# Kernel tuning notes

Measured on AMD Instinct MI355X. Metric: run time of the kernel, lower is better.

## Reference

```python
import jax, jax.numpy as jnp
import numpy as np

N = 100000        # nodes
E = 1600000       # directed edges (avg degree 16)
F_IN, F_HID, F_OUT = 512, 32, 16


def setup_inputs() -> dict:
    key = jax.random.key(0)
    k0, k1, k2, k3 = jax.random.split(key, 4)
    x = jax.random.normal(k0, (N, F_IN), dtype=jnp.float32)
    edge_index = jax.random.randint(k1, (2, E), 0, N, dtype=jnp.int32)
    # Glorot-ish init for the two GCNConv linear weights
    W1 = jax.random.normal(k2, (F_IN, F_HID), dtype=jnp.float32) / np.float32(np.sqrt(F_IN))
    W2 = jax.random.normal(k3, (F_HID, F_OUT), dtype=jnp.float32) / np.float32(np.sqrt(F_HID))
    b1 = jnp.zeros((F_HID,), jnp.float32)
    b2 = jnp.zeros((F_OUT,), jnp.float32)
    return {"x": x, "W1": W1, "b1": b1, "W2": W2, "b2": b2, "edge_index": edge_index}


def gcn_conv(x, W, b, src, dst):
    """PyG GCNConv: h = x W; symmetric-normalized aggregation with self-loops; + bias."""
    h = x @ W                                   # [N, F_out] project first (PyG order)
    # degree including the implicit self-loop (start from ones)
    deg = jnp.ones((N,), h.dtype).at[dst].add(1.0)
    dinv = jax.lax.rsqrt(deg)                   # deg^{-1/2}
    coef = (dinv[src] * dinv[dst])[:, None]     # [E, 1] edge norm
    msg = h[src] * coef                         # gather + scale
    agg = jax.ops.segment_sum(msg, dst, num_segments=N)  # scatter-add to dst
    agg = agg + h * (dinv * dinv)[:, None]      # self-loop contribution
    return agg + b


def reference(x, W1, b1, W2, b2, edge_index):
    src, dst = edge_index[0], edge_index[1]
    h = jax.nn.relu(gcn_conv(x, W1, b1, src, dst))
    # F.dropout(training=self.training) is identity in eval mode
    h = gcn_conv(h, W2, b2, src, dst)
    return jax.nn.log_softmax(h, axis=1)
```

## Files before the change

kernel.cpp:

```cpp
#include <hip/hip_runtime.h>
#include <hip/hip_bf16.h>
#include <cstdint>

#define NN   100000
#define NE   1600000
#define FIN  512
#define FHID 32
#define FOUT 16

#define BSHIFT 8
#define BSIZE  256
#define NBUCK  391
#define EPB    2048
#define NCHUNK ((NE + EPB - 1) / EPB)
#define GROWS  64
#define GB     ((NN + GROWS - 1) / GROWS)

typedef float f32x4 __attribute__((ext_vector_type(4)));
typedef short s16x8 __attribute__((ext_vector_type(8)));
typedef short s16x4 __attribute__((ext_vector_type(4)));
typedef int   i32x4 __attribute__((ext_vector_type(4)));
typedef unsigned int u32;
typedef unsigned short u16;

__device__ __forceinline__ short f2bf(float f) {
  union { float f; uint32_t u; } v; v.f = f;
  uint32_t r = v.u + 0x7fffu + ((v.u >> 16) & 1u);
  return (short)(r >> 16);
}
__device__ __forceinline__ float bf2f(u16 u) {
  union { uint32_t u; float f; } v; v.u = (uint32_t)u << 16; return v.f;
}

__global__ __launch_bounds__(256) void k_hist(const int* __restrict__ dst,
                                              u32* __restrict__ bcount) {
  __shared__ u32 h[NBUCK];
  int tid = threadIdx.x;
  for (int i = tid; i < NBUCK; i += 256) h[i] = 0;
  __syncthreads();
  int base = blockIdx.x * EPB;
  #pragma unroll
  for (int i = 0; i < 2; ++i) {
    int e0 = base + (i * 256 + tid) * 4;
    if (e0 + 3 < NE) {
      i32x4 d4 = *(const i32x4*)(dst + e0);
      atomicAdd(&h[d4[0] >> BSHIFT], 1u);
      atomicAdd(&h[d4[1] >> BSHIFT], 1u);
      atomicAdd(&h[d4[2] >> BSHIFT], 1u);
      atomicAdd(&h[d4[3] >> BSHIFT], 1u);
    } else {
      for (int k = 0; k < 4; ++k)
        if (e0 + k < NE) atomicAdd(&h[dst[e0 + k] >> BSHIFT], 1u);
    }
  }
  __syncthreads();
  for (int i = tid; i < NBUCK; i += 256)
    if (h[i]) atomicAdd(&bcount[i], h[i]);
}

__global__ __launch_bounds__(512) void k_bscan(const u32* __restrict__ bc,
                                               u32* __restrict__ bstart,
                                               u32* __restrict__ bcur,
                                               const float* __restrict__ W1,
                                               u16* __restrict__ wfrag) {
  __shared__ u32 tmp[512];
  int tid = threadIdx.x;
  u32 v = (tid < NBUCK) ? bc[tid] : 0;
  tmp[tid] = v;
  __syncthreads();
  #pragma unroll
  for (int off = 1; off < 512; off <<= 1) {
    u32 t = (tid >= off) ? tmp[tid - off] : 0;
    __syncthreads();
    tmp[tid] += t;
    __syncthreads();
  }
  if (tid < NBUCK) { u32 e = tmp[tid] - v; bstart[tid] = e; bcur[tid] = e; }
  if (tid == 511) bstart[NBUCK] = tmp[511];

  for (int it = 0; it < 32; ++it) {
    int flat = it * 512 + tid;
    int i  = flat & 7;
    int l  = (flat >> 3) & 63;
    int nt = (flat >> 9) & 1;
    int kt = flat >> 10;
    int k  = kt * 32 + ((l >> 4) << 3) + i;
    int n  = nt * 16 + (l & 15);
    wfrag[flat] = (u16)f2bf(W1[k * 32 + n]);
  }
}

__global__ __launch_bounds__(512) void k_bin(const int* __restrict__ src,
                                             const int* __restrict__ dst,
                                             u32* __restrict__ bcur,
                                             u32* __restrict__ binned) {
  __shared__ u32 cnt[NBUCK];
  __shared__ u32 lofs[NBUCK];
  __shared__ u32 gbase[NBUCK];
  __shared__ u32 tmp[512];
  __shared__ u32 stage[EPB];
  __shared__ u16 sb[EPB];
  int tid = threadIdx.x;
  for (int i = tid; i < NBUCK; i += 512) cnt[i] = 0;
  __syncthreads();

  int base = blockIdx.x * EPB;
  int e0 = base + tid * 4;
  u32 vals[4]; u32 ofs[4]; int bks[4];
  if (e0 + 3 < NE) {
    i32x4 s4 = *(const i32x4*)(src + e0);
    i32x4 d4 = *(const i32x4*)(dst + e0);
    #pragma unroll
    for (int k = 0; k < 4; ++k) {
      int b = d4[k] >> BSHIFT;
      bks[k] = b;
      vals[k] = (u32)s4[k] | ((u32)(d4[k] & (BSIZE - 1)) << 17);
      ofs[k] = atomicAdd(&cnt[b], 1u);
    }
  } else {
    #pragma unroll
    for (int k = 0; k < 4; ++k) {
      int e = e0 + k;
      bool ok = e < NE;
      int s = 0, d = 0;
      if (ok) { s = src[e]; d = dst[e]; }
      int b = ok ? (d >> BSHIFT) : -1;
      bks[k] = b;
      vals[k] = (u32)s | ((u32)(d & (BSIZE - 1)) << 17);
      ofs[k] = ok ? atomicAdd(&cnt[b], 1u) : 0;
    }
  }
  __syncthreads();

  u32 cv = (tid < NBUCK) ? cnt[tid] : 0;
  tmp[tid] = cv;
  __syncthreads();
  #pragma unroll
  for (int off = 1; off < 512; off <<= 1) {
    u32 t = (tid >= off) ? tmp[tid - off] : 0;
    __syncthreads();
    tmp[tid] += t;
    __syncthreads();
  }
  if (tid < NBUCK) {
    lofs[tid] = tmp[tid] - cv;
    gbase[tid] = cv ? atomicAdd(&bcur[tid], cv) : 0;
  }
  __syncthreads();
  u32 total = tmp[511];
  __syncthreads();

  #pragma unroll
  for (int k = 0; k < 4; ++k) {
    if (bks[k] >= 0) {
      u32 sl = lofs[bks[k]] + ofs[k];
      stage[sl] = vals[k];
      sb[sl] = (u16)bks[k];
    }
  }
  __syncthreads();

  for (u32 s2 = tid; s2 < total; s2 += 512) {
    int b = sb[s2];
    binned[gbase[b] + (s2 - lofs[b])] = stage[s2];
  }
}

__global__ __launch_bounds__(256) void k_fin(const u32* __restrict__ binned,
                                             const u32* __restrict__ bstart,
                                             int* __restrict__ deg,
                                             int* __restrict__ rs,
                                             float* __restrict__ dinv,
                                             int* __restrict__ csr) {
  __shared__ u32 degl[BSIZE];
  __shared__ u32 rsl[BSIZE];
  int tid = threadIdx.x;
  int b = blockIdx.x;
  u32 start = bstart[b];
  u32 n = bstart[b + 1] - start;

  degl[tid] = 0;
  __syncthreads();
  for (u32 k = tid; k < n; k += 256)
    atomicAdd(&degl[binned[start + k] >> 17], 1u);
  __syncthreads();

  u32 v = degl[tid];
  rsl[tid] = v;
  __syncthreads();
  #pragma unroll
  for (int off = 1; off < 256; off <<= 1) {
    u32 t = (tid >= off) ? rsl[tid - off] : 0;
    __syncthreads();
    rsl[tid] += t;
    __syncthreads();
  }
  u32 e = rsl[tid] - v;
  __syncthreads();
  rsl[tid] = e;

  int g = b * BSIZE + tid;
  if (g < NN) {
    deg[g] = (int)v;
    rs[g] = (int)(start + e);
    dinv[g] = rsqrtf(1.0f + (float)v);
  }
  __syncthreads();

  for (u32 k = tid; k < n; k += 256) {
    u32 vv = binned[start + k];
    u32 pos = atomicAdd(&rsl[vv >> 17], 1u);
    csr[start + pos] = (int)(vv & 0x1FFFFu);
  }
}

__global__ __launch_bounds__(256) void k_gemm1(const float* __restrict__ x,
                                               const u16* __restrict__ wfrag,
                                               const float* __restrict__ dinv,
                                               u16* __restrict__ Hs1) {
  __shared__ u16 Xs[4][16][512];
  const int tid  = threadIdx.x;
  const int lane = tid & 63;
  const int wv   = tid >> 6;
  const int r0   = blockIdx.x * GROWS + wv * 16;
  char* xw = (char*)&Xs[wv][0][0];

  #pragma unroll
  for (int bat = 0; bat < 2; ++bat) {
    f32x4 va[8], vb[8];
    #pragma unroll
    for (int r = 0; r < 8; ++r) {
      int row = r0 + bat * 8 + r;
      if (row >= NN) row = NN - 1;
      const float* rp = x + (size_t)row * FIN;
      va[r] = *(const f32x4*)(rp + lane * 4);
      vb[r] = *(const f32x4*)(rp + 256 + lane * 4);
    }
    #pragma unroll
    for (int r = 0; r < 8; ++r) {
      int rr = bat * 8 + r;
      u32 sw = (u32)((rr & 7) << 4);
      s16x4 w0, w1;
      #pragma unroll
      for (int q = 0; q < 4; ++q) { w0[q] = f2bf(va[r][q]); w1[q] = f2bf(vb[r][q]); }
      *(s16x4*)(xw + (((u32)(rr * 1024 + lane * 8)) ^ sw))       = w0;
      *(s16x4*)(xw + (((u32)(rr * 1024 + 512 + lane * 8)) ^ sw)) = w1;
    }
  }

  const int h = lane >> 4;
  const int m = lane & 15;
  const u32 msw = (u32)((m & 7) << 4);
  const s16x8* wf = (const s16x8*)wfrag;
  f32x4 acc0 = {}, acc1 = {};
  #pragma unroll
  for (int kt = 0; kt < 16; ++kt) {
    s16x8 af = *(const s16x8*)(xw + (((u32)(m * 1024 + kt * 64 + h * 16)) ^ msw));
    s16x8 b0 = wf[(kt * 2 + 0) * 64 + lane];
    s16x8 b1 = wf[(kt * 2 + 1) * 64 + lane];
    acc0 = __builtin_amdgcn_mfma_f32_16x16x32_bf16(af, b0, acc0, 0, 0, 0);
    acc1 = __builtin_amdgcn_mfma_f32_16x16x32_bf16(af, b1, acc1, 0, 0, 0);
  }
  #pragma unroll
  for (int r = 0; r < 4; ++r) {
    int row = r0 + h * 4 + r;
    if (row < NN) {
      float di = dinv[row];
      u16* o = Hs1 + (size_t)row * FHID + m;
      o[0]  = (u16)f2bf(acc0[r] * di);
      o[16] = (u16)f2bf(acc1[r] * di);
    }
  }
}

__global__ __launch_bounds__(256) void k_gat1(const int* __restrict__ csr,
                                              const int* __restrict__ rs,
                                              const int* __restrict__ deg,
                                              const float* __restrict__ dinv,
                                              const float* __restrict__ b1,
                                              const float* __restrict__ W2,
                                              const u16* __restrict__ Hs1,
                                              u16* __restrict__ Hs2) {
  __shared__ float w[FHID * FOUT];
  for (int i = threadIdx.x; i < FHID * FOUT; i += 256) w[i] = W2[i];
  __syncthreads();

  int t = blockIdx.x * 256 + threadIdx.x;
  int d = t >> 2;
  if (d >= NN) return;
  int p = t & 3;
  int start = rs[d], n = deg[d];

  float a0[8], a1[8], a2[8], a3[8];
  {
    s16x8 v = *(const s16x8*)(Hs1 + (size_t)d * FHID + p * 8);
    #pragma unroll
    for (int k = 0; k < 8; ++k) {
      a0[k] = bf2f((u16)v[k]); a1[k] = 0.f; a2[k] = 0.f; a3[k] = 0.f;
    }
  }
  int j = 0;
  for (; j + 8 <= n; j += 8) {
    int s0=csr[start+j],   s1=csr[start+j+1], s2=csr[start+j+2], s3=csr[start+j+3];
    int s4=csr[start+j+4], s5=csr[start+j+5], s6=csr[start+j+6], s7=csr[start+j+7];
    s16x8 v0 = *(const s16x8*)(Hs1 + (size_t)s0 * FHID + p * 8);
    s16x8 v1 = *(const s16x8*)(Hs1 + (size_t)s1 * FHID + p * 8);
    s16x8 v2 = *(const s16x8*)(Hs1 + (size_t)s2 * FHID + p * 8);
    s16x8 v3 = *(const s16x8*)(Hs1 + (size_t)s3 * FHID + p * 8);
    s16x8 v4 = *(const s16x8*)(Hs1 + (size_t)s4 * FHID + p * 8);
    s16x8 v5 = *(const s16x8*)(Hs1 + (size_t)s5 * FHID + p * 8);
    s16x8 v6 = *(const s16x8*)(Hs1 + (size_t)s6 * FHID + p * 8);
    s16x8 v7 = *(const s16x8*)(Hs1 + (size_t)s7 * FHID + p * 8);
    #pragma unroll
    for (int k = 0; k < 8; ++k) {
      a0[k] += bf2f((u16)v0[k]);
      a1[k] += bf2f((u16)v1[k]);
      a2[k] += bf2f((u16)v2[k]);
      a3[k] += bf2f((u16)v3[k]);
      a0[k] += bf2f((u16)v4[k]);
      a1[k] += bf2f((u16)v5[k]);
      a2[k] += bf2f((u16)v6[k]);
      a3[k] += bf2f((u16)v7[k]);
    }
  }
  for (; j + 4 <= n; j += 4) {
    int s0=csr[start+j], s1=csr[start+j+1], s2=csr[start+j+2], s3=csr[start+j+3];
    s16x8 v0 = *(const s16x8*)(Hs1 + (size_t)s0 * FHID + p * 8);
    s16x8 v1 = *(const s16x8*)(Hs1 + (size_t)s1 * FHID + p * 8);
    s16x8 v2 = *(const s16x8*)(Hs1 + (size_t)s2 * FHID + p * 8);
    s16x8 v3 = *(const s16x8*)(Hs1 + (size_t)s3 * FHID + p * 8);
    #pragma unroll
    for (int k = 0; k < 8; ++k) {
      a0[k] += bf2f((u16)v0[k]);
      a1[k] += bf2f((u16)v1[k]);
      a2[k] += bf2f((u16)v2[k]);
      a3[k] += bf2f((u16)v3[k]);
    }
  }
  for (; j < n; ++j) {
    int s0 = csr[start + j];
    s16x8 v0 = *(const s16x8*)(Hs1 + (size_t)s0 * FHID + p * 8);
    #pragma unroll
    for (int k = 0; k < 8; ++k) a0[k] += bf2f((u16)v0[k]);
  }

  float dd = dinv[d];
  float h[8];
  #pragma unroll
  for (int k = 0; k < 8; ++k)
    h[k] = fmaxf(((a0[k] + a1[k]) + (a2[k] + a3[k])) * dd + b1[p * 8 + k], 0.0f);

  float pj[FOUT];
  #pragma unroll
  for (int jj = 0; jj < FOUT; ++jj) pj[jj] = 0.f;
  #pragma unroll
  for (int k = 0; k < 8; ++k)
    #pragma unroll
    for (int jj = 0; jj < FOUT; ++jj)
      pj[jj] = fmaf(h[k], w[(p * 8 + k) * FOUT + jj], pj[jj]);
  #pragma unroll
  for (int jj = 0; jj < FOUT; ++jj) {
    pj[jj] += __shfl_xor(pj[jj], 1);
    pj[jj] += __shfl_xor(pj[jj], 2);
  }
  s16x4 o;
  #pragma unroll
  for (int q = 0; q < 4; ++q) o[q] = f2bf(pj[p * 4 + q] * dd);
  *(s16x4*)(Hs2 + (size_t)d * FOUT + p * 4) = o;
}

__global__ __launch_bounds__(256) void k_gat2(const int* __restrict__ csr,
                                              const int* __restrict__ rs,
                                              const int* __restrict__ deg,
                                              const float* __restrict__ dinv,
                                              const float* __restrict__ b2,
                                              const u16* __restrict__ Hs2,
                                              float* __restrict__ out) {
  int t = blockIdx.x * 256 + threadIdx.x;
  int d = t >> 2;
  if (d >= NN) return;
  int p = t & 3;
  int start = rs[d], n = deg[d];

  float a0[4], a1[4], a2[4], a3[4];
  {
    s16x4 v = *(const s16x4*)(Hs2 + (size_t)d * FOUT + p * 4);
    #pragma unroll
    for (int k = 0; k < 4; ++k) { a0[k] = bf2f((u16)v[k]); a1[k]=0.f; a2[k]=0.f; a3[k]=0.f; }
  }
  int j = 0;
  for (; j + 8 <= n; j += 8) {
    int s0=csr[start+j],   s1=csr[start+j+1], s2=csr[start+j+2], s3=csr[start+j+3];
    int s4=csr[start+j+4], s5=csr[start+j+5], s6=csr[start+j+6], s7=csr[start+j+7];
    s16x4 v0 = *(const s16x4*)(Hs2 + (size_t)s0 * FOUT + p * 4);
    s16x4 v1 = *(const s16x4*)(Hs2 + (size_t)s1 * FOUT + p * 4);
    s16x4 v2 = *(const s16x4*)(Hs2 + (size_t)s2 * FOUT + p * 4);
    s16x4 v3 = *(const s16x4*)(Hs2 + (size_t)s3 * FOUT + p * 4);
    s16x4 v4 = *(const s16x4*)(Hs2 + (size_t)s4 * FOUT + p * 4);
    s16x4 v5 = *(const s16x4*)(Hs2 + (size_t)s5 * FOUT + p * 4);
    s16x4 v6 = *(const s16x4*)(Hs2 + (size_t)s6 * FOUT + p * 4);
    s16x4 v7 = *(const s16x4*)(Hs2 + (size_t)s7 * FOUT + p * 4);
    #pragma unroll
    for (int k = 0; k < 4; ++k) {
      a0[k] += bf2f((u16)v0[k]); a1[k] += bf2f((u16)v1[k]);
      a2[k] += bf2f((u16)v2[k]); a3[k] += bf2f((u16)v3[k]);
      a0[k] += bf2f((u16)v4[k]); a1[k] += bf2f((u16)v5[k]);
      a2[k] += bf2f((u16)v6[k]); a3[k] += bf2f((u16)v7[k]);
    }
  }
  for (; j + 4 <= n; j += 4) {
    int s0=csr[start+j], s1=csr[start+j+1], s2=csr[start+j+2], s3=csr[start+j+3];
    s16x4 v0 = *(const s16x4*)(Hs2 + (size_t)s0 * FOUT + p * 4);
    s16x4 v1 = *(const s16x4*)(Hs2 + (size_t)s1 * FOUT + p * 4);
    s16x4 v2 = *(const s16x4*)(Hs2 + (size_t)s2 * FOUT + p * 4);
    s16x4 v3 = *(const s16x4*)(Hs2 + (size_t)s3 * FOUT + p * 4);
    #pragma unroll
    for (int k = 0; k < 4; ++k) {
      a0[k] += bf2f((u16)v0[k]); a1[k] += bf2f((u16)v1[k]);
      a2[k] += bf2f((u16)v2[k]); a3[k] += bf2f((u16)v3[k]);
    }
  }
  for (; j < n; ++j) {
    int s0 = csr[start + j];
    s16x4 v0 = *(const s16x4*)(Hs2 + (size_t)s0 * FOUT + p * 4);
    #pragma unroll
    for (int k = 0; k < 4; ++k) a0[k] += bf2f((u16)v0[k]);
  }

  float dd = dinv[d];
  float z[4];
  #pragma unroll
  for (int k = 0; k < 4; ++k)
    z[k] = ((a0[k]+a1[k]) + (a2[k]+a3[k])) * dd + b2[p * 4 + k];

  float m = fmaxf(fmaxf(z[0], z[1]), fmaxf(z[2], z[3]));
  m = fmaxf(m, __shfl_xor(m, 1));
  m = fmaxf(m, __shfl_xor(m, 2));
  float s = expf(z[0]-m) + expf(z[1]-m) + expf(z[2]-m) + expf(z[3]-m);
  s += __shfl_xor(s, 1);
  s += __shfl_xor(s, 2);
  float lse = m + logf(s);

  f32x4 o = { z[0]-lse, z[1]-lse, z[2]-lse, z[3]-lse };
  *(f32x4*)(out + (size_t)d * FOUT + p * 4) = o;
}

extern "C" void kernel_launch(void* const* d_in, const int* in_sizes, int n_in,
                              void* d_out, int out_size, void* d_ws, size_t ws_size,
                              hipStream_t stream) {
  const float* x  = (const float*)d_in[0];
  const float* W1 = (const float*)d_in[1];
  const float* b1 = (const float*)d_in[2];
  const float* W2 = (const float*)d_in[3];
  const float* b2 = (const float*)d_in[4];
  const int*   ei = (const int*)d_in[5];
  const int* srcv = ei;
  const int* dstv = ei + NE;

  char* ws = (char*)d_ws;
  const size_t KB = 1024, MB = 1048576;
  u32*   bcount = (u32*)(ws + 0);
  u32*   bstart = (u32*)(ws + 8 * KB);
  u32*   bcur   = (u32*)(ws + 16 * KB);
  u16*   wfrag  = (u16*)(ws + 64 * KB);
  int*   deg    = (int*)(ws + 512 * KB);
  int*   rs     = (int*)(ws + 1024 * KB);
  float* dinv   = (float*)(ws + 1536 * KB);
  u32*   binned = (u32*)(ws + 2 * MB);
  int*   csr    = (int*)(ws + 9 * MB);
  u16*   Hs1    = (u16*)(ws + 16 * MB);
  u16*   Hs2    = (u16*)(ws + 23 * MB);
  float* out    = (float*)d_out;

  hipMemsetAsync(bcount, 0, NBUCK * sizeof(u32), stream);

  k_hist <<<NCHUNK, 256, 0, stream>>>(dstv, bcount);
  k_bscan<<<1,      512, 0, stream>>>(bcount, bstart, bcur, W1, wfrag);
  k_bin  <<<NCHUNK, 512, 0, stream>>>(srcv, dstv, bcur, binned);
  k_fin  <<<NBUCK,  256, 0, stream>>>(binned, bstart, deg, rs, dinv, csr);
  k_gemm1<<<GB, 256, 0, stream>>>(x, wfrag, dinv, Hs1);
  k_gat1 <<<(NN * 4 + 255) / 256, 256, 0, stream>>>(csr, rs, deg, dinv, b1, W2, Hs1, Hs2);
  k_gat2 <<<(NN * 4 + 255) / 256, 256, 0, stream>>>(csr, rs, deg, dinv, b2, Hs2, out);
}
```

Measured before the change: 155.2 us.

## Pipeline GEMM1 tiles per wave and enlarge histogram/binning work per block

The feature GEMM now has each wave process two 16-row tiles: it issues the global loads for the second tile before running MFMA on the first, so memory latency overlaps compute, and the grid halves to 782 blocks. The histogram becomes a grid-stride loop over 128 blocks, cutting the number of global atomic merges. Binning handles 4096 edges per block with 8 edges per thread, giving fewer blocks and fewer global bucket-cursor atomics. The costs are higher register pressure in GEMM (16+16 f32x4 held live), more shared memory in binning, and less parallelism in the histogram. The histogram loop also drops the tail path, which is only safe because NE is a multiple of 4.

Measured after the change: 139.2 us. 10.3% less time.

```diff
diff --git a/kernel.cpp b/kernel.cpp
--- a/kernel.cpp
+++ b/kernel.cpp
@@ -11,10 +11,10 @@
 #define BSHIFT 8
 #define BSIZE  256
 #define NBUCK  391
-#define EPB    2048
-#define NCHUNK ((NE + EPB - 1) / EPB)
-#define GROWS  64
-#define GB     ((NN + GROWS - 1) / GROWS)
+#define HB     128
+#define BEPB   4096
+#define NBB    ((NE + BEPB - 1) / BEPB)
+#define GB     782
 
 typedef float f32x4 __attribute__((ext_vector_type(4)));
 typedef short s16x8 __attribute__((ext_vector_type(8)));
@@ -38,20 +38,13 @@
   int tid = threadIdx.x;
   for (int i = tid; i < NBUCK; i += 256) h[i] = 0;
   __syncthreads();
-  int base = blockIdx.x * EPB;
-  #pragma unroll
-  for (int i = 0; i < 2; ++i) {
-    int e0 = base + (i * 256 + tid) * 4;
-    if (e0 + 3 < NE) {
-      i32x4 d4 = *(const i32x4*)(dst + e0);
-      atomicAdd(&h[d4[0] >> BSHIFT], 1u);
-      atomicAdd(&h[d4[1] >> BSHIFT], 1u);
-      atomicAdd(&h[d4[2] >> BSHIFT], 1u);
-      atomicAdd(&h[d4[3] >> BSHIFT], 1u);
-    } else {
-      for (int k = 0; k < 4; ++k)
-        if (e0 + k < NE) atomicAdd(&h[dst[e0 + k] >> BSHIFT], 1u);
-    }
+  const int stride = HB * 256 * 4;
+  for (int e0 = (blockIdx.x * 256 + tid) * 4; e0 + 3 < NE; e0 += stride) {
+    i32x4 d4 = *(const i32x4*)(dst + e0);
+    atomicAdd(&h[d4[0] >> BSHIFT], 1u);
+    atomicAdd(&h[d4[1] >> BSHIFT], 1u);
+    atomicAdd(&h[d4[2] >> BSHIFT], 1u);
+    atomicAdd(&h[d4[3] >> BSHIFT], 1u);
   }
   __syncthreads();
   for (int i = tid; i < NBUCK; i += 256)
@@ -98,36 +91,39 @@
   __shared__ u32 lofs[NBUCK];
   __shared__ u32 gbase[NBUCK];
   __shared__ u32 tmp[512];
-  __shared__ u32 stage[EPB];
-  __shared__ u16 sb[EPB];
+  __shared__ u32 stage[BEPB];
+  __shared__ u16 sb[BEPB];
   int tid = threadIdx.x;
   for (int i = tid; i < NBUCK; i += 512) cnt[i] = 0;
   __syncthreads();
 
-  int base = blockIdx.x * EPB;
-  int e0 = base + tid * 4;
-  u32 vals[4]; u32 ofs[4]; int bks[4];
-  if (e0 + 3 < NE) {
-    i32x4 s4 = *(const i32x4*)(src + e0);
-    i32x4 d4 = *(const i32x4*)(dst + e0);
-    #pragma unroll
-    for (int k = 0; k < 4; ++k) {
-      int b = d4[k] >> BSHIFT;
-      bks[k] = b;
-      vals[k] = (u32)s4[k] | ((u32)(d4[k] & (BSIZE - 1)) << 17);
-      ofs[k] = atomicAdd(&cnt[b], 1u);
-    }
-  } else {
-    #pragma unroll
-    for (int k = 0; k < 4; ++k) {
-      int e = e0 + k;
-      bool ok = e < NE;
-      int s = 0, d = 0;
-      if (ok) { s = src[e]; d = dst[e]; }
-      int b = ok ? (d >> BSHIFT) : -1;
-      bks[k] = b;
-      vals[k] = (u32)s | ((u32)(d & (BSIZE - 1)) << 17);
-      ofs[k] = ok ? atomicAdd(&cnt[b], 1u) : 0;
+  int base = blockIdx.x * BEPB;
+  u32 vals[8]; u32 ofs[8]; int bks[8];
+  #pragma unroll
+  for (int half = 0; half < 2; ++half) {
+    int e0 = base + tid * 8 + half * 4;
+    if (e0 + 3 < NE) {
+      i32x4 s4 = *(const i32x4*)(src + e0);
+      i32x4 d4 = *(const i32x4*)(dst + e0);
+      #pragma unroll
+      for (int k = 0; k < 4; ++k) {
+        int b = d4[k] >> BSHIFT;
+        bks[half * 4 + k] = b;
+        vals[half * 4 + k] = (u32)s4[k] | ((u32)(d4[k] & (BSIZE - 1)) << 17);
+        ofs[half * 4 + k] = atomicAdd(&cnt[b], 1u);
+      }
+    } else {
+      #pragma unroll
+      for (int k = 0; k < 4; ++k) {
+        int e = e0 + k;
+        bool ok = e < NE;
+        int s = 0, d = 0;
+        if (ok) { s = src[e]; d = dst[e]; }
+        int b = ok ? (d >> BSHIFT) : -1;
+        bks[half * 4 + k] = b;
+        vals[half * 4 + k] = (u32)s | ((u32)(d & (BSIZE - 1)) << 17);
+        ofs[half * 4 + k] = ok ? atomicAdd(&cnt[b], 1u) : 0;
+      }
     }
   }
   __syncthreads();
@@ -151,7 +147,7 @@
   __syncthreads();
 
   #pragma unroll
-  for (int k = 0; k < 4; ++k) {
+  for (int k = 0; k < 8; ++k) {
     if (bks[k] >= 0) {
       u32 sl = lofs[bks[k]] + ofs[k];
       stage[sl] = vals[k];
@@ -214,6 +210,60 @@
   }
 }
 
+#define G1_ISSUE(TILE)                                                        \
+  do {                                                                        \
+    int r0_ = (TILE) * 16;                                                    \
+    _Pragma("unroll")                                                         \
+    for (int r_ = 0; r_ < 16; ++r_) {                                         \
+      int row_ = r0_ + r_;                                                    \
+      if (row_ >= NN) row_ = NN - 1;                                          \
+      const float* rp_ = x + (size_t)row_ * FIN + lane * 4;                   \
+      va[r_] = *(const f32x4*)rp_;                                            \
+      vb[r_] = *(const f32x4*)(rp_ + 256);                                    \
+    }                                                                         \
+  } while (0)
+
+#define G1_CVTWRITE()                                                         \
+  do {                                                                        \
+    _Pragma("unroll")                                                         \
+    for (int r_ = 0; r_ < 16; ++r_) {                                         \
+      u32 sw_ = (u32)((r_ & 7) << 4);                                         \
+      s16x4 w0_, w1_;                                                         \
+      _Pragma("unroll")                                                       \
+      for (int q_ = 0; q_ < 4; ++q_) {                                        \
+        w0_[q_] = f2bf(va[r_][q_]);                                           \
+        w1_[q_] = f2bf(vb[r_][q_]);                                           \
+      }                                                                       \
+      *(s16x4*)(xw + (((u32)(r_ * 1024 + lane * 8)) ^ sw_)) = w0_;            \
+      *(s16x4*)(xw + (((u32)(r_ * 1024 + 512 + lane * 8)) ^ sw_)) = w1_;      \
+    }                                                                         \
+  } while (0)
+
+#define G1_MFMA_STORE(TILE)                                                   \
+  do {                                                                        \
+    f32x4 acc0_ = {}, acc1_ = {};                                             \
+    _Pragma("unroll")                                                         \
+    for (int kt_ = 0; kt_ < 16; ++kt_) {                                      \
+      s16x8 af_ = *(const s16x8*)(xw +                                        \
+          (((u32)(m * 1024 + kt_ * 64 + h * 16)) ^ msw));                     \
+      s16x8 b0_ = wf[(kt_ * 2 + 0) * 64 + lane];                              \
+      s16x8 b1_ = wf[(kt_ * 2 + 1) * 64 + lane];                              \
+      acc0_ = __builtin_amdgcn_mfma_f32_16x16x32_bf16(af_, b0_, acc0_, 0,0,0);\
+      acc1_ = __builtin_amdgcn_mfma_f32_16x16x32_bf16(af_, b1_, acc1_, 0,0,0);\
+    }                                                                         \
+    int r0_ = (TILE) * 16;                                                    \
+    _Pragma("unroll")                                                         \
+    for (int r_ = 0; r_ < 4; ++r_) {                                          \
+      int row_ = r0_ + h * 4 + r_;                                            \
+      if (row_ < NN) {                                                        \
+        float di_ = dinv[row_];                                               \
+        u16* o_ = Hs1 + (size_t)row_ * FHID + m;                              \
+        o_[0]  = (u16)f2bf(acc0_[r_] * di_);                                  \
+        o_[16] = (u16)f2bf(acc1_[r_] * di_);                                  \
+      }                                                                       \
+    }                                                                         \
+  } while (0)
+
 __global__ __launch_bounds__(256) void k_gemm1(const float* __restrict__ x,
                                                const u16* __restrict__ wfrag,
                                                const float* __restrict__ dinv,
@@ -222,55 +272,21 @@
   const int tid  = threadIdx.x;
   const int lane = tid & 63;
   const int wv   = tid >> 6;
-  const int r0   = blockIdx.x * GROWS + wv * 16;
   char* xw = (char*)&Xs[wv][0][0];
-
-  #pragma unroll
-  for (int bat = 0; bat < 2; ++bat) {
-    f32x4 va[8], vb[8];
-    #pragma unroll
-    for (int r = 0; r < 8; ++r) {
-      int row = r0 + bat * 8 + r;
-      if (row >= NN) row = NN - 1;
-      const float* rp = x + (size_t)row * FIN;
-      va[r] = *(const f32x4*)(rp + lane * 4);
-      vb[r] = *(const f32x4*)(rp + 256 + lane * 4);
-    }
-    #pragma unroll
-    for (int r = 0; r < 8; ++r) {
-      int rr = bat * 8 + r;
-      u32 sw = (u32)((rr & 7) << 4);
-      s16x4 w0, w1;
-      #pragma unroll
-      for (int q = 0; q < 4; ++q) { w0[q] = f2bf(va[r][q]); w1[q] = f2bf(vb[r][q]); }
-      *(s16x4*)(xw + (((u32)(rr * 1024 + lane * 8)) ^ sw))       = w0;
-      *(s16x4*)(xw + (((u32)(rr * 1024 + 512 + lane * 8)) ^ sw)) = w1;
-    }
-  }
-
   const int h = lane >> 4;
   const int m = lane & 15;
   const u32 msw = (u32)((m & 7) << 4);
   const s16x8* wf = (const s16x8*)wfrag;
-  f32x4 acc0 = {}, acc1 = {};
-  #pragma unroll
-  for (int kt = 0; kt < 16; ++kt) {
-    s16x8 af = *(const s16x8*)(xw + (((u32)(m * 1024 + kt * 64 + h * 16)) ^ msw));
-    s16x8 b0 = wf[(kt * 2 + 0) * 64 + lane];
-    s16x8 b1 = wf[(kt * 2 + 1) * 64 + lane];
-    acc0 = __builtin_amdgcn_mfma_f32_16x16x32_bf16(af, b0, acc0, 0, 0, 0);
-    acc1 = __builtin_amdgcn_mfma_f32_16x16x32_bf16(af, b1, acc1, 0, 0, 0);
-  }
-  #pragma unroll
-  for (int r = 0; r < 4; ++r) {
-    int row = r0 + h * 4 + r;
-    if (row < NN) {
-      float di = dinv[row];
-      u16* o = Hs1 + (size_t)row * FHID + m;
-      o[0]  = (u16)f2bf(acc0[r] * di);
-      o[16] = (u16)f2bf(acc1[r] * di);
-    }
-  }
+
+  const int t0 = (blockIdx.x * 4 + wv) * 2;
+  f32x4 va[16], vb[16];
+
+  G1_ISSUE(t0);
+  G1_CVTWRITE();
+  G1_ISSUE(t0 + 1);
+  G1_MFMA_STORE(t0);
+  G1_CVTWRITE();
+  G1_MFMA_STORE(t0 + 1);
 }
 
 __global__ __launch_bounds__(256) void k_gat1(const int* __restrict__ csr,
@@ -474,10 +490,10 @@
 
   hipMemsetAsync(bcount, 0, NBUCK * sizeof(u32), stream);
 
-  k_hist <<<NCHUNK, 256, 0, stream>>>(dstv, bcount);
-  k_bscan<<<1,      512, 0, stream>>>(bcount, bstart, bcur, W1, wfrag);
-  k_bin  <<<NCHUNK, 512, 0, stream>>>(srcv, dstv, bcur, binned);
-  k_fin  <<<NBUCK,  256, 0, stream>>>(binned, bstart, deg, rs, dinv, csr);
+  k_hist <<<HB,  256, 0, stream>>>(dstv, bcount);
+  k_bscan<<<1,   512, 0, stream>>>(bcount, bstart, bcur, W1, wfrag);
+  k_bin  <<<NBB, 512, 0, stream>>>(srcv, dstv, bcur, binned);
+  k_fin  <<<NBUCK, 256, 0, stream>>>(binned, bstart, deg, rs, dinv, csr);
   k_gemm1<<<GB, 256, 0, stream>>>(x, wfrag, dinv, Hs1);
   k_gat1 <<<(NN * 4 + 255) / 256, 256, 0, stream>>>(csr, rs, deg, dinv, b1, W2, Hs1, Hs2);
   k_gat2 <<<(NN * 4 + 255) / 256, 256, 0, stream>>>(csr, rs, deg, dinv, b2, Hs2, out);
```
